# Kernel optimization log

Measured on AMD Instinct MI355X. Metric: run time of the kernel, lower is better.

Reference implementation:

```python
import jax, jax.numpy as jnp
import numpy as np

E, DEPTH, H, T_BLOCK, VOC = 1024, 8, 16, 2048, 256
DH = E // H
B, T = 4, 2048
EPS = 1e-5


def _layernorm(x, g, b):
    mu = jnp.mean(x, axis=-1, keepdims=True)
    var = jnp.mean(jnp.square(x - mu), axis=-1, keepdims=True)
    return (x - mu) * jax.lax.rsqrt(var + EPS) * g + b


def setup_inputs() -> dict:
    key = jax.random.key(0)
    ks = iter(jax.random.split(key, 32))

    def xav(k, shape):
        fan_in, fan_out = shape[-2], shape[-1]
        lim = np.sqrt(6.0 / (fan_in + fan_out))
        return jax.random.uniform(k, shape, jnp.float32, -lim, lim)

    inp = {
        "tokens": jax.random.randint(next(ks), (B, T), 0, VOC),
        "emb_w": xav(next(ks), (VOC, E)),
        "pos_w": xav(next(ks), (T_BLOCK, E)),
        # per-layer stacked params
        "Wq": xav(next(ks), (DEPTH, H, E, DH)),
        "Wk": xav(next(ks), (DEPTH, H, E, DH)),
        "Wv": xav(next(ks), (DEPTH, H, E, DH)),
        "Wo": xav(next(ks), (DEPTH, E, E)),        # stored [in, out]
        "ln1_g": jnp.ones((DEPTH, E)), "ln1_b": jnp.zeros((DEPTH, E)),
        "W1": xav(next(ks), (DEPTH, E, 4 * E)), "b1": jnp.zeros((DEPTH, 4 * E)),
        "W2": xav(next(ks), (DEPTH, 4 * E, E)), "b2": jnp.zeros((DEPTH, E)),
        "ln2_g": jnp.ones((DEPTH, E)), "ln2_b": jnp.zeros((DEPTH, E)),
        "lnf_g": jnp.ones((E,)), "lnf_b": jnp.zeros((E,)),
        "Wu": xav(next(ks), (E, 2)), "bu": jnp.zeros((2,)),
    }
    return inp


def _forward(tokens, emb_w, pos_w, Wq, Wk, Wv, Wo, ln1_g, ln1_b,
             W1, b1, W2, b2, ln2_g, ln2_b, lnf_g, lnf_b, Wu, bu):
    Tlen = tokens.shape[1]
    x = emb_w[tokens] + pos_w[:Tlen]                       # [B, T, E]
    scale = 1.0 / jnp.sqrt(jnp.float32(Tlen))              # NOTE: original divides by sqrt(seq_len)
    for l in range(Wq.shape[0]):
        h = _layernorm(x, ln1_g[l], ln1_b[l])
        q = jnp.einsum('hed,bte->bhtd', Wq[l], h)
        k = jnp.einsum('hed,bte->bhtd', Wk[l], h)
        v = jnp.einsum('hed,bte->bhtd', Wv[l], h)
        scores = jnp.einsum('bhtd,bhsd->bhts', q, k) * scale
        attn = jax.nn.softmax(scores, axis=-1)
        att = jnp.einsum('bhts,bhsd->bhtd', attn, v)       # [B, H, T, DH]
        att = att.transpose(0, 2, 1, 3).reshape(x.shape)   # b t (h d)
        x = x + att @ Wo[l]
        h = _layernorm(x, ln2_g[l], ln2_b[l])
        x = x + jax.nn.relu(h @ W1[l] + b1[l]) @ W2[l] + b2[l]
    x = _layernorm(x, lnf_g, lnf_b)
    return x @ Wu + bu                                     # [B, T, 2]


def reference(tokens, emb_w, pos_w, Wq, Wk, Wv, Wo, ln1_g, ln1_b,
              W1, b1, W2, b2, ln2_g, ln2_b, lnf_g, lnf_b, Wu, bu):
    return _forward(tokens, emb_w, pos_w, Wq, Wk, Wv, Wo, ln1_g, ln1_b,
                    W1, b1, W2, b2, ln2_g, ln2_b, lnf_g, lnf_b, Wu, bu)
```

## Files before the change

kernel.cpp:

```cpp
#include <hip/hip_runtime.h>
#include <hip/hip_bf16.h>
#include <math.h>

#define E_DIM 1024
#define T_SEQ 2048
#define NH 16
#define DHEAD 64
#define NB 4
#define NLAYER 8

typedef __attribute__((ext_vector_type(8))) short bf16x8;
typedef __attribute__((ext_vector_type(4))) short short4v;
typedef __attribute__((ext_vector_type(4))) float f32x4;

static __device__ __forceinline__ short f2bf(float f) {
  union { __hip_bfloat16 h; short s; } u;
  u.h = __float2bfloat16(f);
  return u.s;
}
static __device__ __forceinline__ float bf2f(short s) {
  union { unsigned u; float f; } v;
  v.u = ((unsigned)(unsigned short)s) << 16;
  return v.f;
}

__global__ __launch_bounds__(256) void embed_kernel(const int* __restrict__ tokens,
    const float* __restrict__ emb, const float* __restrict__ pos, float* __restrict__ x) {
  int idx = blockIdx.x * 256 + threadIdx.x;
  int bt = idx >> 10;
  int e  = idx & 1023;
  int t  = bt & (T_SEQ - 1);
  int tok = tokens[bt];
  x[idx] = emb[tok * E_DIM + e] + pos[t * E_DIM + e];
}

__global__ __launch_bounds__(256) void ln_bf16_kernel(const float* __restrict__ x,
    const float* __restrict__ g, const float* __restrict__ b, short* __restrict__ out) {
  __shared__ float s1[4], s2[4];
  int row = blockIdx.x;
  const float4* xr = (const float4*)(x + (size_t)row * E_DIM);
  float4 xv = xr[threadIdx.x];
  float s = xv.x + xv.y + xv.z + xv.w;
  float q = xv.x*xv.x + xv.y*xv.y + xv.z*xv.z + xv.w*xv.w;
  #pragma unroll
  for (int off = 32; off; off >>= 1) {
    s += __shfl_xor(s, off, 64);
    q += __shfl_xor(q, off, 64);
  }
  int lane = threadIdx.x & 63, wid = threadIdx.x >> 6;
  if (lane == 0) { s1[wid] = s; s2[wid] = q; }
  __syncthreads();
  float mean = (s1[0] + s1[1] + s1[2] + s1[3]) * (1.0f / E_DIM);
  float ms   = (s2[0] + s2[1] + s2[2] + s2[3]) * (1.0f / E_DIM);
  float rstd = rsqrtf(ms - mean * mean + 1e-5f);
  float4 gv = ((const float4*)g)[threadIdx.x];
  float4 bv = ((const float4*)b)[threadIdx.x];
  short4v ov;
  ov.x = f2bf((xv.x - mean) * rstd * gv.x + bv.x);
  ov.y = f2bf((xv.y - mean) * rstd * gv.y + bv.y);
  ov.z = f2bf((xv.z - mean) * rstd * gv.z + bv.z);
  ov.w = f2bf((xv.w - mean) * rstd * gv.w + bv.w);
  *(short4v*)(out + (size_t)row * E_DIM + threadIdx.x * 4) = ov;
}

__global__ void castT_kernel(const float* __restrict__ in, short* __restrict__ out,
                             int K, int N) {
  __shared__ float tile[32][33];
  int k0 = blockIdx.x * 32, n0 = blockIdx.y * 32;
  const float* ib = in + (size_t)blockIdx.z * K * N;
  short* ob = out + (size_t)blockIdx.z * N * K;
  int tx = threadIdx.x, ty = threadIdx.y;
  #pragma unroll
  for (int i = 0; i < 4; ++i)
    tile[ty + 8 * i][tx] = ib[(size_t)(k0 + ty + 8 * i) * N + n0 + tx];
  __syncthreads();
  #pragma unroll
  for (int i = 0; i < 4; ++i)
    ob[(size_t)(n0 + ty + 8 * i) * K + k0 + tx] = f2bf(tile[tx][ty + 8 * i]);
}

struct GemmP {
  const short* A; const short* B; void* C;
  const float* bias; const float* res;
  long sAb, sAt, sAh;
  long sBh, sBd;
  long sCb, sCt, sCh;
  int K; float alpha; int relu; int cbf16; int hasbias; int hasres;
};

__global__ __launch_bounds__(256) void gemm_bf16(GemmP p) {
  __shared__ __align__(16) short As[128 * 64];
  __shared__ __align__(16) short Bs[128 * 64];
  const int t = threadIdx.x;
  const int lane = t & 63, wid = t >> 6;
  const int wr = wid >> 1, wc = wid & 1;
  const long bm = (long)blockIdx.y * 128, bn = (long)blockIdx.x * 128;

  const int prow = t >> 3;
  const int pcol = t & 7;
  long aRow[4], bRow[4];
  int wIdx[4];
  #pragma unroll
  for (int c = 0; c < 4; ++c) {
    int r = c * 32 + prow;
    long gm = bm + r, gn = bn + r;
    aRow[c] = (gm >> 11) * p.sAb + (gm & 2047) * p.sAt;
    bRow[c] = (gn >> 6) * p.sBh + (gn & 63) * p.sBd;
    wIdx[c] = r * 64 + ((pcol ^ (r & 7)) << 3);
  }

  const int rA = lane & 15;
  const int g  = lane >> 4;
  int aOff[4][2], bOff[4][2];
  #pragma unroll
  for (int f = 0; f < 4; ++f) {
    int rowa = wr * 64 + f * 16 + rA;
    int rowb = wc * 64 + f * 16 + rA;
    #pragma unroll
    for (int kk = 0; kk < 2; ++kk) {
      aOff[f][kk] = rowa * 64 + (((g + kk * 4) ^ (rowa & 7)) << 3);
      bOff[f][kk] = rowb * 64 + (((g + kk * 4) ^ (rowb & 7)) << 3);
    }
  }

  f32x4 acc[4][4] = {};
  bf16x8 ra[4], rb[4];
  {
    long kc = (long)(pcol * 8);
    long ka = (kc >> 6) * p.sAh + (kc & 63);
    #pragma unroll
    for (int c = 0; c < 4; ++c) {
      ra[c] = *(const bf16x8*)(p.A + aRow[c] + ka);
      rb[c] = *(const bf16x8*)(p.B + bRow[c] + kc);
    }
  }

  for (int k0 = 0; k0 < p.K; k0 += 64) {
    __syncthreads();
    #pragma unroll
    for (int c = 0; c < 4; ++c) {
      *(bf16x8*)&As[wIdx[c]] = ra[c];
      *(bf16x8*)&Bs[wIdx[c]] = rb[c];
    }
    __syncthreads();
    if (k0 + 64 < p.K) {
      long kc = (long)(k0 + 64 + pcol * 8);
      long ka = (kc >> 6) * p.sAh + (kc & 63);
      #pragma unroll
      for (int c = 0; c < 4; ++c) {
        ra[c] = *(const bf16x8*)(p.A + aRow[c] + ka);
        rb[c] = *(const bf16x8*)(p.B + bRow[c] + kc);
      }
    }
    #pragma unroll
    for (int kk = 0; kk < 2; ++kk) {
      bf16x8 af[4], bf[4];
      #pragma unroll
      for (int f = 0; f < 4; ++f) {
        af[f] = *(const bf16x8*)&As[aOff[f][kk]];
        bf[f] = *(const bf16x8*)&Bs[bOff[f][kk]];
      }
      #pragma unroll
      for (int i = 0; i < 4; ++i)
        #pragma unroll
        for (int j = 0; j < 4; ++j)
          acc[i][j] = __builtin_amdgcn_mfma_f32_16x16x32_bf16(af[i], bf[j], acc[i][j], 0, 0, 0);
    }
  }

  float bias4[4];
  long ncol[4];
  #pragma unroll
  for (int j = 0; j < 4; ++j) {
    long n = bn + wc * 64 + j * 16 + rA;
    ncol[j] = (n >> 6) * p.sCh + (n & 63);
    bias4[j] = p.hasbias ? p.bias[n] : 0.f;
  }
  #pragma unroll
  for (int i = 0; i < 4; ++i) {
    #pragma unroll
    for (int r = 0; r < 4; ++r) {
      long m = bm + wr * 64 + i * 16 + g * 4 + r;
      long mb = (m >> 11) * p.sCb + (m & 2047) * p.sCt;
      #pragma unroll
      for (int j = 0; j < 4; ++j) {
        long ca = mb + ncol[j];
        float v = p.alpha * acc[i][j][r] + bias4[j];
        if (p.relu) v = fmaxf(v, 0.f);
        if (p.hasres) v += p.res[ca];
        if (p.cbf16) ((short*)p.C)[ca] = f2bf(v);
        else ((float*)p.C)[ca] = v;
      }
    }
  }
}

__global__ __launch_bounds__(512) void attn_mfma_kernel(const short* __restrict__ qkv,
                                                        short* __restrict__ att) {
  __shared__ __align__(16) short Ks[64 * 64];
  __shared__ __align__(16) short Vt[64 * 64];
  __shared__ __align__(16) short Pq[8 * 16 * 64];

  const int t = threadIdx.x;
  const int lane = t & 63, wid = t >> 6;
  const int bh = blockIdx.x >> 4;
  const int b = bh >> 4, h = bh & 15;
  const int q0blk = (blockIdx.x & 15) * 128;
  const int rA = lane & 15;
  const int g  = lane >> 4;
  const int xq = (rA & 7) << 3;
  const float scale = 0.022097086912079608f;

  const short* Qg = qkv + (size_t)b * 6291456 + (size_t)h * 131072;
  const short* Kg = Qg + 2097152;
  const short* Vg = Qg + 4194304;

  const int q0w = q0blk + wid * 16;
  bf16x8 qf0 = *(const bf16x8*)(Qg + (size_t)(q0w + rA) * DHEAD + g * 8);
  bf16x8 qf1 = *(const bf16x8*)(Qg + (size_t)(q0w + rA) * DHEAD + 32 + g * 8);

  short* Pw = Pq + wid * 1024;
  const int ss = t >> 3, sp = t & 7;

  float mrun = -1e30f, lrun = 0.f;
  f32x4 acco[4] = {};

  bf16x8 kreg = *(const bf16x8*)(Kg + (size_t)ss * DHEAD + sp * 8);
  bf16x8 vreg = *(const bf16x8*)(Vg + (size_t)ss * DHEAD + sp * 8);

  for (int tile = 0; tile < T_SEQ / 64; ++tile) {
    __syncthreads();
    *(bf16x8*)&Ks[ss * 64 + ((sp ^ (ss & 7)) << 3)] = kreg;
    #pragma unroll
    for (int j = 0; j < 8; ++j) {
      int d = sp * 8 + j;
      Vt[d * 64 + ((ss + 8 * (sp + j)) & 63)] = vreg[j];
    }
    __syncthreads();
    if (tile + 1 < T_SEQ / 64) {
      kreg = *(const bf16x8*)(Kg + (size_t)((tile + 1) * 64 + ss) * DHEAD + sp * 8);
      vreg = *(const bf16x8*)(Vg + (size_t)((tile + 1) * 64 + ss) * DHEAD + sp * 8);
    }

    f32x4 accs[4];
    __builtin_amdgcn_s_setprio(1);
    #pragma unroll
    for (int st = 0; st < 4; ++st) {
      int srow = st * 16 + rA;
      bf16x8 kf0 = *(const bf16x8*)&Ks[srow * 64 + ((g ^ (rA & 7)) << 3)];
      bf16x8 kf1 = *(const bf16x8*)&Ks[srow * 64 + (((g + 4) ^ (rA & 7)) << 3)];
      f32x4 z = {};
      z = __builtin_amdgcn_mfma_f32_16x16x32_bf16(kf0, qf0, z, 0, 0, 0);
      accs[st] = __builtin_amdgcn_mfma_f32_16x16x32_bf16(kf1, qf1, z, 0, 0, 0);
    }
    __builtin_amdgcn_s_setprio(0);

    float tm = -1e30f;
    #pragma unroll
    for (int st = 0; st < 4; ++st) {
      #pragma unroll
      for (int r = 0; r < 4; ++r) {
        accs[st][r] *= scale;
        tm = fmaxf(tm, accs[st][r]);
      }
    }
    tm = fmaxf(tm, __shfl_xor(tm, 16));
    tm = fmaxf(tm, __shfl_xor(tm, 32));
    float mnew = fmaxf(mrun, tm);
    float ts = 0.f;
    float pv[16];
    #pragma unroll
    for (int st = 0; st < 4; ++st)
      #pragma unroll
      for (int r = 0; r < 4; ++r) {
        float e = __expf(accs[st][r] - mnew);
        pv[st * 4 + r] = e;
        ts += e;
      }
    ts += __shfl_xor(ts, 16);
    ts += __shfl_xor(ts, 32);
    float corr = __expf(mrun - mnew);
    lrun = lrun * corr + ts;
    mrun = mnew;

    #pragma unroll
    for (int st = 0; st < 4; ++st) {
      short4v pk;
      pk.x = f2bf(pv[st * 4 + 0]);
      pk.y = f2bf(pv[st * 4 + 1]);
      pk.z = f2bf(pv[st * 4 + 2]);
      pk.w = f2bf(pv[st * 4 + 3]);
      *(short4v*)&Pw[(rA * 64 + st * 16 + g * 4) ^ xq] = pk;
    }
    asm volatile("s_waitcnt lgkmcnt(0)" ::: "memory");

    float c4r[4];
    #pragma unroll
    for (int r = 0; r < 4; ++r) c4r[r] = __shfl(corr, g * 4 + r);
    #pragma unroll
    for (int dt = 0; dt < 4; ++dt)
      #pragma unroll
      for (int r = 0; r < 4; ++r) acco[dt][r] *= c4r[r];

    __builtin_amdgcn_s_setprio(1);
    #pragma unroll
    for (int sk = 0; sk < 2; ++sk) {
      bf16x8 pf = *(const bf16x8*)&Pw[(rA * 64 + sk * 32 + g * 8) ^ xq];
      #pragma unroll
      for (int dt = 0; dt < 4; ++dt) {
        int d = dt * 16 + rA;
        bf16x8 vf = *(const bf16x8*)&Vt[d * 64 +
            ((sk * 32 + g * 8 + 8 * (dt * 2 + (rA >> 3) + (rA & 7))) & 63)];
        acco[dt] = __builtin_amdgcn_mfma_f32_16x16x32_bf16(pf, vf, acco[dt], 0, 0, 0);
      }
    }
    __builtin_amdgcn_s_setprio(0);
  }

  float l4[4];
  #pragma unroll
  for (int r = 0; r < 4; ++r) l4[r] = 1.0f / __shfl(lrun, g * 4 + r);
  #pragma unroll
  for (int dt = 0; dt < 4; ++dt)
    #pragma unroll
    for (int r = 0; r < 4; ++r)
      att[(size_t)bh * T_SEQ * DHEAD + (size_t)(q0w + g * 4 + r) * DHEAD + dt * 16 + rA] =
          f2bf(acco[dt][r] * l4[r]);
}

__global__ __launch_bounds__(256) void head_kernel(const short* __restrict__ h,
    const float* __restrict__ Wu, const float* __restrict__ bu, float* __restrict__ out) {
  __shared__ float sm[8];
  int row = blockIdx.x;
  const short* hr = h + (size_t)row * E_DIM;
  float a0 = 0.f, a1 = 0.f;
  for (int i = threadIdx.x; i < E_DIM; i += 256) {
    float hv = bf2f(hr[i]);
    a0 = fmaf(hv, Wu[i * 2 + 0], a0);
    a1 = fmaf(hv, Wu[i * 2 + 1], a1);
  }
  #pragma unroll
  for (int off = 32; off; off >>= 1) {
    a0 += __shfl_xor(a0, off, 64);
    a1 += __shfl_xor(a1, off, 64);
  }
  int lane = threadIdx.x & 63, wid = threadIdx.x >> 6;
  if (lane == 0) { sm[wid] = a0; sm[4 + wid] = a1; }
  __syncthreads();
  if (threadIdx.x == 0) {
    out[row * 2 + 0] = sm[0] + sm[1] + sm[2] + sm[3] + bu[0];
    out[row * 2 + 1] = sm[4] + sm[5] + sm[6] + sm[7] + bu[1];
  }
}

static inline void launch_gemm(hipStream_t stream, int N,
    const short* A, long sAb, long sAt, long sAh,
    const short* B, long sBh, long sBd,
    void* C, long sCb, long sCt, long sCh,
    const float* bias, const float* res, int K, float alpha,
    int relu, int cbf16) {
  GemmP p;
  p.A = A; p.B = B; p.C = C; p.bias = bias; p.res = res;
  p.sAb = sAb; p.sAt = sAt; p.sAh = sAh;
  p.sBh = sBh; p.sBd = sBd;
  p.sCb = sCb; p.sCt = sCt; p.sCh = sCh;
  p.K = K; p.alpha = alpha; p.relu = relu; p.cbf16 = cbf16;
  p.hasbias = bias != nullptr; p.hasres = res != nullptr;
  dim3 grid(N / 128, (NB * T_SEQ) / 128);
  gemm_bf16<<<grid, 256, 0, stream>>>(p);
}

extern "C" void kernel_launch(void* const* d_in, const int* in_sizes, int n_in,
                              void* d_out, int out_size, void* d_ws, size_t ws_size,
                              hipStream_t stream) {
  const int*   tokens = (const int*)d_in[0];
  const float* emb_w  = (const float*)d_in[1];
  const float* pos_w  = (const float*)d_in[2];
  const float* Wq     = (const float*)d_in[3];
  const float* Wk     = (const float*)d_in[4];
  const float* Wv     = (const float*)d_in[5];
  const float* Wo     = (const float*)d_in[6];
  const float* ln1_g  = (const float*)d_in[7];
  const float* ln1_b  = (const float*)d_in[8];
  const float* W1     = (const float*)d_in[9];
  const float* b1     = (const float*)d_in[10];
  const float* W2     = (const float*)d_in[11];
  const float* b2     = (const float*)d_in[12];
  const float* ln2_g  = (const float*)d_in[13];
  const float* ln2_b  = (const float*)d_in[14];
  const float* lnf_g  = (const float*)d_in[15];
  const float* lnf_b  = (const float*)d_in[16];
  const float* Wu     = (const float*)d_in[17];
  const float* bu     = (const float*)d_in[18];
  float* out = (float*)d_out;

  char* ws = (char*)d_ws;
  float* X     = (float*)(ws);
  short* Hb    = (short*)(ws + 33554432);
  short* QKVb  = (short*)(ws + 50331648);
  short* FFH   = (short*)(ws + 100663296);
  short* WqkvT = (short*)(ws + 167772160);
  short* WoT   = (short*)(ws + 174063616);
  short* W1T   = (short*)(ws + 176160768);
  short* W2T   = (short*)(ws + 184549376);

  embed_kernel<<<32768, 256, 0, stream>>>(tokens, emb_w, pos_w, X);

  dim3 tb(32, 8);
  for (int l = 0; l < NLAYER; ++l) {
    castT_kernel<<<dim3(32, 2, 16), tb, 0, stream>>>(Wq + (size_t)l * 1048576, WqkvT, 1024, 64);
    castT_kernel<<<dim3(32, 2, 16), tb, 0, stream>>>(Wk + (size_t)l * 1048576, WqkvT + 1048576, 1024, 64);
    castT_kernel<<<dim3(32, 2, 16), tb, 0, stream>>>(Wv + (size_t)l * 1048576, WqkvT + 2097152, 1024, 64);
    castT_kernel<<<dim3(32, 32, 1), tb, 0, stream>>>(Wo + (size_t)l * 1048576, WoT, 1024, 1024);
    castT_kernel<<<dim3(32, 128, 1), tb, 0, stream>>>(W1 + (size_t)l * 4194304, W1T, 1024, 4096);
    castT_kernel<<<dim3(128, 32, 1), tb, 0, stream>>>(W2 + (size_t)l * 4194304, W2T, 4096, 1024);

    ln_bf16_kernel<<<8192, 256, 0, stream>>>(X, ln1_g + l * 1024, ln1_b + l * 1024, Hb);

    launch_gemm(stream, 3072, Hb, 2097152, 1024, 64, WqkvT, 65536, 1024,
                QKVb, 6291456, 64, 131072, nullptr, nullptr, 1024, 1.0f, 0, 1);

    attn_mfma_kernel<<<1024, 512, 0, stream>>>(QKVb, Hb);

    launch_gemm(stream, 1024, Hb, 2097152, 64, 131072, WoT, 65536, 1024,
                X, 2097152, 1024, 64, nullptr, X, 1024, 1.0f, 0, 0);

    ln_bf16_kernel<<<8192, 256, 0, stream>>>(X, ln2_g + l * 1024, ln2_b + l * 1024, Hb);

    launch_gemm(stream, 4096, Hb, 2097152, 1024, 64, W1T, 65536, 1024,
                FFH, 8388608, 4096, 64, b1 + (size_t)l * 4096, nullptr, 1024, 1.0f, 1, 1);
    launch_gemm(stream, 1024, FFH, 8388608, 4096, 64, W2T, 262144, 4096,
                X, 2097152, 1024, 64, b2 + (size_t)l * 1024, X, 4096, 1.0f, 0, 0);
  }

  ln_bf16_kernel<<<8192, 256, 0, stream>>>(X, lnf_g, lnf_b, Hb);
  head_kernel<<<8192, 256, 0, stream>>>(Hb, Wu, bu, out);
}
```

Before: 3.651 ms.

## Fuse weight casts, swizzle workgroups across XCDs, fold scale into Q, lazy softmax rescale

Merges the six per-layer weight cast/transpose launches into one prep kernel. Remaps the GEMM and attention workgroup indices so neighbouring tiles land on the same XCD, for better L2 reuse. Folds the attention scale into the Q projection epilogue and switches softmax to exp2. The running max and output accumulator are now rescaled only when the max rises by more than a threshold. The lazy rescale defers the row-sum reduction to the end and relies on bounded growth of the exponentials to stay numerically safe.

```diff
diff --git a/kernel.cpp b/kernel.cpp
--- a/kernel.cpp
+++ b/kernel.cpp
@@ -13,6 +13,12 @@
 typedef __attribute__((ext_vector_type(4))) short short4v;
 typedef __attribute__((ext_vector_type(4))) float f32x4;
 
+#if __has_builtin(__builtin_amdgcn_exp2f)
+#define EXP2(x) __builtin_amdgcn_exp2f(x)
+#else
+#define EXP2(x) exp2f(x)
+#endif
+
 static __device__ __forceinline__ short f2bf(float f) {
   union { __hip_bfloat16 h; short s; } u;
   u.h = __float2bfloat16(f);
@@ -22,6 +28,10 @@
   union { unsigned u; float f; } v;
   v.u = ((unsigned)(unsigned short)s) << 16;
   return v.f;
+}
+
+static __device__ __forceinline__ int xcd_swz(int orig, int nwg) {
+  return (orig & 7) * (nwg >> 3) + (orig >> 3);
 }
 
 __global__ __launch_bounds__(256) void embed_kernel(const int* __restrict__ tokens,
@@ -63,20 +73,34 @@
   *(short4v*)(out + (size_t)row * E_DIM + threadIdx.x * 4) = ov;
 }
 
-__global__ void castT_kernel(const float* __restrict__ in, short* __restrict__ out,
-                             int K, int N) {
+struct PrepP {
+  const float *s0, *s1, *s2, *s3, *s4, *s5;
+  short *d0, *d1, *d2, *d3, *d4, *d5;
+};
+
+__global__ void prep_kernel(PrepP p) {
   __shared__ float tile[32][33];
-  int k0 = blockIdx.x * 32, n0 = blockIdx.y * 32;
-  const float* ib = in + (size_t)blockIdx.z * K * N;
-  short* ob = out + (size_t)blockIdx.z * N * K;
+  int bid = blockIdx.x;
+  const float* src; short* dst; int K, N, kb, local;
+  if (bid < 1024)      { src = p.s0; dst = p.d0; K = 1024; N = 64;   kb = 32;  local = bid; }
+  else if (bid < 2048) { src = p.s1; dst = p.d1; K = 1024; N = 64;   kb = 32;  local = bid - 1024; }
+  else if (bid < 3072) { src = p.s2; dst = p.d2; K = 1024; N = 64;   kb = 32;  local = bid - 2048; }
+  else if (bid < 4096) { src = p.s3; dst = p.d3; K = 1024; N = 1024; kb = 32;  local = bid - 3072; }
+  else if (bid < 8192) { src = p.s4; dst = p.d4; K = 1024; N = 4096; kb = 32;  local = bid - 4096; }
+  else                 { src = p.s5; dst = p.d5; K = 4096; N = 1024; kb = 128; local = bid - 8192; }
+  int per = kb * (N >> 5);
+  int z = local / per, rem = local % per;
+  int k0 = (rem % kb) * 32, n0 = (rem / kb) * 32;
+  src += (size_t)z * K * N;
+  dst += (size_t)z * N * K;
   int tx = threadIdx.x, ty = threadIdx.y;
   #pragma unroll
   for (int i = 0; i < 4; ++i)
-    tile[ty + 8 * i][tx] = ib[(size_t)(k0 + ty + 8 * i) * N + n0 + tx];
+    tile[ty + 8 * i][tx] = src[(size_t)(k0 + ty + 8 * i) * N + n0 + tx];
   __syncthreads();
   #pragma unroll
   for (int i = 0; i < 4; ++i)
-    ob[(size_t)(n0 + ty + 8 * i) * K + k0 + tx] = f2bf(tile[tx][ty + 8 * i]);
+    dst[(size_t)(n0 + ty + 8 * i) * K + k0 + tx] = f2bf(tile[tx][ty + 8 * i]);
 }
 
 struct GemmP {
@@ -85,7 +109,8 @@
   long sAb, sAt, sAh;
   long sBh, sBd;
   long sCb, sCt, sCh;
-  int K; float alpha; int relu; int cbf16; int hasbias; int hasres;
+  int K; float alpha; int alphaN; int gridx;
+  int relu; int cbf16; int hasbias; int hasres;
 };
 
 __global__ __launch_bounds__(256) void gemm_bf16(GemmP p) {
@@ -94,7 +119,8 @@
   const int t = threadIdx.x;
   const int lane = t & 63, wid = t >> 6;
   const int wr = wid >> 1, wc = wid & 1;
-  const long bm = (long)blockIdx.y * 128, bn = (long)blockIdx.x * 128;
+  const int wg = xcd_swz(blockIdx.x, gridDim.x);
+  const long bm = (long)(wg / p.gridx) * 128, bn = (long)(wg % p.gridx) * 128;
 
   const int prow = t >> 3;
   const int pcol = t & 7;
@@ -168,13 +194,14 @@
     }
   }
 
-  float bias4[4];
+  float bias4[4], aa4[4];
   long ncol[4];
   #pragma unroll
   for (int j = 0; j < 4; ++j) {
     long n = bn + wc * 64 + j * 16 + rA;
     ncol[j] = (n >> 6) * p.sCh + (n & 63);
     bias4[j] = p.hasbias ? p.bias[n] : 0.f;
+    aa4[j] = (n < p.alphaN) ? p.alpha : 1.0f;
   }
   #pragma unroll
   for (int i = 0; i < 4; ++i) {
@@ -185,7 +212,7 @@
       #pragma unroll
       for (int j = 0; j < 4; ++j) {
         long ca = mb + ncol[j];
-        float v = p.alpha * acc[i][j][r] + bias4[j];
+        float v = aa4[j] * acc[i][j][r] + bias4[j];
         if (p.relu) v = fmaxf(v, 0.f);
         if (p.hasres) v += p.res[ca];
         if (p.cbf16) ((short*)p.C)[ca] = f2bf(v);
@@ -203,13 +230,14 @@
 
   const int t = threadIdx.x;
   const int lane = t & 63, wid = t >> 6;
-  const int bh = blockIdx.x >> 4;
+  const int wg = xcd_swz(blockIdx.x, gridDim.x);
+  const int bh = wg >> 4;
   const int b = bh >> 4, h = bh & 15;
-  const int q0blk = (blockIdx.x & 15) * 128;
+  const int q0blk = (wg & 15) * 128;
   const int rA = lane & 15;
   const int g  = lane >> 4;
   const int xq = (rA & 7) << 3;
-  const float scale = 0.022097086912079608f;
+  const float L2E = 1.4426950408889634f;
 
   const short* Qg = qkv + (size_t)b * 6291456 + (size_t)h * 131072;
   const short* Kg = Qg + 2097152;
@@ -255,33 +283,50 @@
     }
     __builtin_amdgcn_s_setprio(0);
 
-    float tm = -1e30f;
-    #pragma unroll
-    for (int st = 0; st < 4; ++st) {
-      #pragma unroll
-      for (int r = 0; r < 4; ++r) {
-        accs[st][r] *= scale;
-        tm = fmaxf(tm, accs[st][r]);
-      }
-    }
+    float tm = accs[0][0];
+    #pragma unroll
+    for (int st = 0; st < 4; ++st)
+      #pragma unroll
+      for (int r = 0; r < 4; ++r) tm = fmaxf(tm, accs[st][r]);
     tm = fmaxf(tm, __shfl_xor(tm, 16));
     tm = fmaxf(tm, __shfl_xor(tm, 32));
-    float mnew = fmaxf(mrun, tm);
-    float ts = 0.f;
+
     float pv[16];
-    #pragma unroll
-    for (int st = 0; st < 4; ++st)
-      #pragma unroll
-      for (int r = 0; r < 4; ++r) {
-        float e = __expf(accs[st][r] - mnew);
-        pv[st * 4 + r] = e;
-        ts += e;
-      }
-    ts += __shfl_xor(ts, 16);
-    ts += __shfl_xor(ts, 32);
-    float corr = __expf(mrun - mnew);
-    lrun = lrun * corr + ts;
-    mrun = mnew;
+    if (__all(tm - mrun <= 8.0f)) {
+      float mL = mrun * L2E;
+      float ts = 0.f;
+      #pragma unroll
+      for (int st = 0; st < 4; ++st)
+        #pragma unroll
+        for (int r = 0; r < 4; ++r) {
+          float e = EXP2(fmaf(accs[st][r], L2E, -mL));
+          pv[st * 4 + r] = e;
+          ts += e;
+        }
+      lrun += ts;
+    } else {
+      float mnew = fmaxf(mrun, tm);
+      float mL = mnew * L2E;
+      float corr = EXP2((mrun - mnew) * L2E);
+      float ts = 0.f;
+      #pragma unroll
+      for (int st = 0; st < 4; ++st)
+        #pragma unroll
+        for (int r = 0; r < 4; ++r) {
+          float e = EXP2(fmaf(accs[st][r], L2E, -mL));
+          pv[st * 4 + r] = e;
+          ts += e;
+        }
+      lrun = lrun * corr + ts;
+      mrun = mnew;
+      float c4r[4];
+      #pragma unroll
+      for (int r = 0; r < 4; ++r) c4r[r] = __shfl(corr, g * 4 + r);
+      #pragma unroll
+      for (int dt = 0; dt < 4; ++dt)
+        #pragma unroll
+        for (int r = 0; r < 4; ++r) acco[dt][r] *= c4r[r];
+    }
 
     #pragma unroll
     for (int st = 0; st < 4; ++st) {
@@ -294,14 +339,6 @@
     }
     asm volatile("s_waitcnt lgkmcnt(0)" ::: "memory");
 
-    float c4r[4];
-    #pragma unroll
-    for (int r = 0; r < 4; ++r) c4r[r] = __shfl(corr, g * 4 + r);
-    #pragma unroll
-    for (int dt = 0; dt < 4; ++dt)
-      #pragma unroll
-      for (int r = 0; r < 4; ++r) acco[dt][r] *= c4r[r];
-
     __builtin_amdgcn_s_setprio(1);
     #pragma unroll
     for (int sk = 0; sk < 2; ++sk) {
@@ -317,6 +354,8 @@
     __builtin_amdgcn_s_setprio(0);
   }
 
+  lrun += __shfl_xor(lrun, 16);
+  lrun += __shfl_xor(lrun, 32);
   float l4[4];
   #pragma unroll
   for (int r = 0; r < 4; ++r) l4[r] = 1.0f / __shfl(lrun, g * 4 + r);
@@ -357,17 +396,18 @@
     const short* A, long sAb, long sAt, long sAh,
     const short* B, long sBh, long sBd,
     void* C, long sCb, long sCt, long sCh,
-    const float* bias, const float* res, int K, float alpha,
+    const float* bias, const float* res, int K, float alpha, int alphaN,
     int relu, int cbf16) {
   GemmP p;
   p.A = A; p.B = B; p.C = C; p.bias = bias; p.res = res;
   p.sAb = sAb; p.sAt = sAt; p.sAh = sAh;
   p.sBh = sBh; p.sBd = sBd;
   p.sCb = sCb; p.sCt = sCt; p.sCh = sCh;
-  p.K = K; p.alpha = alpha; p.relu = relu; p.cbf16 = cbf16;
+  p.K = K; p.alpha = alpha; p.alphaN = alphaN; p.gridx = N / 128;
+  p.relu = relu; p.cbf16 = cbf16;
   p.hasbias = bias != nullptr; p.hasres = res != nullptr;
-  dim3 grid(N / 128, (NB * T_SEQ) / 128);
-  gemm_bf16<<<grid, 256, 0, stream>>>(p);
+  int nwg = (N / 128) * ((NB * T_SEQ) / 128);
+  gemm_bf16<<<nwg, 256, 0, stream>>>(p);
 }
 
 extern "C" void kernel_launch(void* const* d_in, const int* in_sizes, int n_in,
@@ -404,33 +444,36 @@
   short* W1T   = (short*)(ws + 176160768);
   short* W2T   = (short*)(ws + 184549376);
 
+  const float scale = 0.022097086912079608f;
+
   embed_kernel<<<32768, 256, 0, stream>>>(tokens, emb_w, pos_w, X);
 
-  dim3 tb(32, 8);
   for (int l = 0; l < NLAYER; ++l) {
-    castT_kernel<<<dim3(32, 2, 16), tb, 0, stream>>>(Wq + (size_t)l * 1048576, WqkvT, 1024, 64);
-    castT_kernel<<<dim3(32, 2, 16), tb, 0, stream>>>(Wk + (size_t)l * 1048576, WqkvT + 1048576, 1024, 64);
-    castT_kernel<<<dim3(32, 2, 16), tb, 0, stream>>>(Wv + (size_t)l * 1048576, WqkvT + 2097152, 1024, 64);
-    castT_kernel<<<dim3(32, 32, 1), tb, 0, stream>>>(Wo + (size_t)l * 1048576, WoT, 1024, 1024);
-    castT_kernel<<<dim3(32, 128, 1), tb, 0, stream>>>(W1 + (size_t)l * 4194304, W1T, 1024, 4096);
-    castT_kernel<<<dim3(128, 32, 1), tb, 0, stream>>>(W2 + (size_t)l * 4194304, W2T, 4096, 1024);
+    PrepP pp;
+    pp.s0 = Wq + (size_t)l * 1048576; pp.d0 = WqkvT;
+    pp.s1 = Wk + (size_t)l * 1048576; pp.d1 = WqkvT + 1048576;
+    pp.s2 = Wv + (size_t)l * 1048576; pp.d2 = WqkvT + 2097152;
+    pp.s3 = Wo + (size_t)l * 1048576; pp.d3 = WoT;
+    pp.s4 = W1 + (size_t)l * 4194304; pp.d4 = W1T;
+    pp.s5 = W2 + (size_t)l * 4194304; pp.d5 = W2T;
+    prep_kernel<<<12288, dim3(32, 8), 0, stream>>>(pp);
 
     ln_bf16_kernel<<<8192, 256, 0, stream>>>(X, ln1_g + l * 1024, ln1_b + l * 1024, Hb);
 
     launch_gemm(stream, 3072, Hb, 2097152, 1024, 64, WqkvT, 65536, 1024,
-                QKVb, 6291456, 64, 131072, nullptr, nullptr, 1024, 1.0f, 0, 1);
+                QKVb, 6291456, 64, 131072, nullptr, nullptr, 1024, scale, 1024, 0, 1);
 
     attn_mfma_kernel<<<1024, 512, 0, stream>>>(QKVb, Hb);
 
     launch_gemm(stream, 1024, Hb, 2097152, 64, 131072, WoT, 65536, 1024,
-                X, 2097152, 1024, 64, nullptr, X, 1024, 1.0f, 0, 0);
+                X, 2097152, 1024, 64, nullptr, X, 1024, 1.0f, 0, 0, 0);
 
     ln_bf16_kernel<<<8192, 256, 0, stream>>>(X, ln2_g + l * 1024, ln2_b + l * 1024, Hb);
 
     launch_gemm(stream, 4096, Hb, 2097152, 1024, 64, W1T, 65536, 1024,
-                FFH, 8388608, 4096, 64, b1 + (size_t)l * 4096, nullptr, 1024, 1.0f, 1, 1);
+                FFH, 8388608, 4096, 64, b1 + (size_t)l * 4096, nullptr, 1024, 1.0f, 0, 1, 1);
     launch_gemm(stream, 1024, FFH, 8388608, 4096, 64, W2T, 262144, 4096,
-                X, 2097152, 1024, 64, b2 + (size_t)l * 1024, X, 4096, 1.0f, 0, 0);
+                X, 2097152, 1024, 64, b2 + (size_t)l * 1024, X, 4096, 1.0f, 0, 0, 0);
   }
 
   ln_bf16_kernel<<<8192, 256, 0, stream>>>(X, lnf_g, lnf_b, Hb);
```

Result: faster. 3.442 ms (-5.7%).
